# Kernel tuning notes

Hardware: AMD Instinct MI355X
Metric: run time of the kernel (lower is better)

Reference implementation:

```python
import jax, jax.numpy as jnp
import numpy as np

T, N, I, H, OUT = 16, 4096, 4, 32, 1


def setup_inputs() -> dict:
    key = jax.random.key(0)
    ks = jax.random.split(key, 12)
    f32 = jnp.float32
    x_path = jax.random.normal(ks[0], (T, N, I), f32)
    adj = jax.random.normal(ks[1], (N, N), f32) / np.float32(np.sqrt(N))
    W_enc = jax.random.normal(ks[2], (I, H), f32) / np.float32(np.sqrt(I))
    b_enc = jnp.zeros((H,), f32)
    W_gcn = jax.random.normal(ks[3], (H, H), f32) / np.float32(np.sqrt(H))
    b_gcn = jnp.zeros((H,), f32)
    W_time = jax.random.normal(ks[4], (H, H), f32) / np.float32(np.sqrt(H))
    b_time = jnp.zeros((H,), f32)
    W_proj = jax.random.normal(ks[5], (H, H * I), f32) * np.float32(0.1 / np.sqrt(H))
    b_proj = jnp.zeros((H * I,), f32)
    W_d1 = jax.random.normal(ks[6], (H, 16), f32) / np.float32(np.sqrt(H))
    b_d1 = jnp.zeros((16,), f32)
    W_d2 = jax.random.normal(ks[7], (16, OUT), f32) / np.float32(4.0)
    b_d2 = jnp.zeros((OUT,), f32)
    return dict(x_path=x_path, adj=adj, W_enc=W_enc, b_enc=b_enc,
                W_gcn=W_gcn, b_gcn=b_gcn, W_time=W_time, b_time=b_time,
                W_proj=W_proj, b_proj=b_proj, W_d1=W_d1, b_d1=b_d1,
                W_d2=W_d2, b_d2=b_d2)


def _natural_cubic_coeffs(y):
    # y: (T, C) samples on uniform grid t=0..T-1 (h=1).
    # Natural cubic spline: tridiagonal solve for second derivatives M.
    Tn = y.shape[0]
    main = jnp.ones((Tn,), y.dtype).at[1:-1].set(4.0)
    A = jnp.diag(main)
    idx = jnp.arange(1, Tn - 1)
    A = A.at[idx, idx - 1].set(1.0).at[idx, idx + 1].set(1.0)
    rhs = jnp.zeros_like(y).at[1:-1].set(6.0 * (y[2:] - 2.0 * y[1:-1] + y[:-2]))
    M = jnp.linalg.solve(A, rhs)
    b = (y[1:] - y[:-1]) - (2.0 * M[:-1] + M[1:]) / 6.0
    c = M[:-1] / 2.0
    d = (M[1:] - M[:-1]) / 6.0
    return b, c, d  # each (T-1, C); dX/dt on interval i at local s: b+2cs+3ds^2


def reference(x_path, adj, W_enc, b_enc, W_gcn, b_gcn, W_time, b_time,
              W_proj, b_proj, W_d1, b_d1, W_d2, b_d2):
    Tn, Nn, In = x_path.shape
    Hn = W_enc.shape[1]
    y = x_path.reshape(Tn, Nn * In)
    sb, sc, sd = _natural_cubic_coeffs(y)

    # z0 = encoder(X(t0)); spline value at grid point 0 equals the sample.
    z0 = x_path[0] @ W_enc + b_enc  # (N, H)

    def vf(z, dxdt):
        # SpatialVectorField + projector + block-diagonal Jacobian applied to dX/dt.
        # z: (N, H), dxdt: (N, I)
        zn = adj @ z                                     # GCN neighbor aggregation
        h = jax.nn.relu(zn @ W_gcn + b_gcn + z @ W_time + b_time)
        sens = (h @ W_proj + b_proj).reshape(Nn, Hn, In)  # per-site Jacobian blocks
        # site_identity * sens -> block-diag; matmul with dX reduces to per-site contraction
        return jnp.einsum('nhi,ni->nh', sens, dxdt)

    def rk4_step(z, coefs):
        bi, ci, di = coefs  # (N*I,)
        def dxdt(s):
            return (bi + 2.0 * ci * s + 3.0 * di * s * s).reshape(Nn, In)
        k1 = vf(z, dxdt(0.0))
        k2 = vf(z + 0.5 * k1, dxdt(0.5))
        k3 = vf(z + 0.5 * k2, dxdt(0.5))
        k4 = vf(z + k3, dxdt(1.0))
        zn = z + (k1 + 2.0 * k2 + 2.0 * k3 + k4) / 6.0
        return zn, zn

    _, zs = jax.lax.scan(rk4_step, z0, (sb, sc, sd))
    zT = jnp.concatenate([z0[None], zs], axis=0)  # (T, N, H)

    hdec = jax.nn.relu(zT @ W_d1 + b_d1)
    return jax.nn.sigmoid(hdec @ W_d2 + b_d2)  # (T, N, OUT)
```

## Files before the change

### kernel.cpp

```cpp
#include <hip/hip_runtime.h>
#include <hip/hip_bf16.h>

#define NN 4096
#define NI 16384
#define HH 32

typedef __attribute__((ext_vector_type(8))) short short8;
typedef __attribute__((ext_vector_type(4))) float f32x4;

__device__ __forceinline__ short f2bs(float f) {
  __hip_bfloat16 b = __float2bfloat16(f);
  return *(short*)&b;
}

__device__ __forceinline__ unsigned pack2(float lo, float hi) {
  return (unsigned)(unsigned short)f2bs(lo) |
         ((unsigned)(unsigned short)f2bs(hi) << 16);
}

__device__ __forceinline__ long zt_idx(int n, int h) {
  const int hb = h >> 4, hl = h & 15;
  const int kb = n >> 5, oct = (n >> 3) & 3, j = n & 7;
  return ((long)(hb * 128 + kb) * 64 + hl + 16 * oct) * 8 + j;
}

__global__ void k_spline(const float* __restrict__ x,
                         float* __restrict__ dx0, float* __restrict__ dxh,
                         float* __restrict__ dx1, unsigned* __restrict__ bar) {
  if (blockIdx.x == 0) {
    for (int i = threadIdx.x; i < 576; i += 256) bar[i] = 0u;
  }
  const int c = blockIdx.x * 256 + threadIdx.x;
  float y[16];
#pragma unroll
  for (int t = 0; t < 16; ++t) y[t] = x[t * NI + c];
  float cp[15], dp[15], M[16];
  cp[1] = 0.25f;
  dp[1] = (6.f * (y[2] - 2.f * y[1] + y[0])) * 0.25f;
#pragma unroll
  for (int i = 2; i <= 14; ++i) {
    float ri = 6.f * (y[i + 1] - 2.f * y[i] + y[i - 1]);
    float inv = 1.f / (4.f - cp[i - 1]);
    cp[i] = inv;
    dp[i] = (ri - dp[i - 1]) * inv;
  }
  M[0] = 0.f; M[15] = 0.f;
  M[14] = dp[14];
#pragma unroll
  for (int i = 13; i >= 1; --i) M[i] = dp[i] - cp[i] * M[i + 1];
#pragma unroll
  for (int i = 0; i < 15; ++i) {
    float b = (y[i + 1] - y[i]) - (2.f * M[i] + M[i + 1]) * (1.f / 6.f);
    float cc = 0.5f * M[i];
    float dd = (M[i + 1] - M[i]) * (1.f / 6.f);
    dx0[i * NI + c] = b;
    dxh[i * NI + c] = b + cc + 0.75f * dd;
    dx1[i * NI + c] = b + 2.f * cc + 3.f * dd;
  }
}

__device__ __forceinline__ void gridbar(unsigned* bar, int bid, int e) {
  __syncthreads();
  if (threadIdx.x == 0) {
    asm volatile("s_waitcnt vmcnt(0)" ::: "memory");
    unsigned old = __hip_atomic_fetch_add(bar + (bid & 7) * 32, 1u,
                                          __ATOMIC_RELAXED, __HIP_MEMORY_SCOPE_AGENT);
    if (old == (unsigned)(32 * e - 1)) {
      unsigned rr = __hip_atomic_fetch_add(bar + 256, 1u,
                                           __ATOMIC_RELAXED, __HIP_MEMORY_SCOPE_AGENT);
      if (rr == (unsigned)(8 * e - 1)) {
#pragma unroll
        for (int g = 0; g < 8; ++g)
          __hip_atomic_store(bar + 320 + g * 32, (unsigned)e,
                             __ATOMIC_RELAXED, __HIP_MEMORY_SCOPE_AGENT);
      }
    }
    while (__hip_atomic_load(bar + 320 + (bid & 7) * 32, __ATOMIC_RELAXED,
                             __HIP_MEMORY_SCOPE_AGENT) < (unsigned)e)
      __builtin_amdgcn_s_sleep(8);
    __builtin_amdgcn_fence(__ATOMIC_ACQUIRE, "agent");
  }
  __syncthreads();
}

__device__ __forceinline__ void dec_block(const float* zsrc ,
                                          const float* Wd1s ,
                                          const float* dsm, float* op,
                                          int r0, int tid) {
  if (tid < 256) {
    const int rr = tid >> 4, jj = tid & 15;
    float hv = dsm[jj];
#pragma unroll
    for (int hh = 0; hh < 32; ++hh) hv = fmaf(zsrc[rr * 33 + hh], Wd1s[hh * 16 + jj], hv);
    float val = fmaxf(hv, 0.f) * dsm[16 + jj];
#pragma unroll
    for (int off = 1; off < 16; off <<= 1) val += __shfl_xor(val, off, 64);
    if (jj == 0)
      __hip_atomic_store(op + r0 + rr, 1.f / (1.f + expf(-(dsm[32] + val))),
                         __ATOMIC_RELAXED, __HIP_MEMORY_SCOPE_AGENT);
  }
}

__global__ __launch_bounds__(1024, 4) void k_ode(
    const float* __restrict__ adj, const float* __restrict__ x,
    const float* __restrict__ dx0, const float* __restrict__ dxh,
    const float* __restrict__ dx1,
    const float* __restrict__ We, const float* __restrict__ be,
    const float* __restrict__ Wg, const float* __restrict__ bg,
    const float* __restrict__ Wt, const float* __restrict__ bt,
    const float* __restrict__ Wp, const float* __restrict__ bp,
    const float* __restrict__ Wd1, const float* __restrict__ bd1,
    const float* __restrict__ Wd2, const float* __restrict__ bd2,
    short* __restrict__ zTa, short* __restrict__ zTb,
    unsigned* __restrict__ bar, float* __restrict__ out) {
  __shared__ float red2[16][32][17];
  __shared__ float zn_s[16][33];
  __shared__ float h_s[16][33];
  __shared__ float ze_s[16][33];
  __shared__ float zb_s[16][33];
  __shared__ float ka_s[16][33];
  __shared__ float Wg_s[32][32];
  __shared__ float Wt_s[32][32];
  __shared__ float Wp_s[32][136];
  __shared__ float Wd1_s[32][16];
  __shared__ float bgt_s[32];
  __shared__ float bp_s[128];
  __shared__ float dsm[33];

  const int tid = threadIdx.x;
  const int lane = tid & 63;
  const int w = tid >> 6;
  const int bid = blockIdx.x;
  const int r0 = bid * 16;
  const int lane8 = lane * 8;
  const int fr = lane & 15, oct = lane >> 4;

  short8 av[8];
  {
    const float* arow = adj + (long)(r0 + fr) * NN + w * 256 + oct * 8;
#pragma unroll
    for (int i = 0; i < 8; ++i) {
      const float4 u0 = *(const float4*)(arow + i * 32);
      const float4 u1 = *(const float4*)(arow + i * 32 + 4);
      short8 rf;
      rf[0] = f2bs(u0.x); rf[1] = f2bs(u0.y); rf[2] = f2bs(u0.z); rf[3] = f2bs(u0.w);
      rf[4] = f2bs(u1.x); rf[5] = f2bs(u1.y); rf[6] = f2bs(u1.z); rf[7] = f2bs(u1.w);
      av[i] = rf;
    }
  }

  Wg_s[tid >> 5][tid & 31] = Wg[tid];
  Wt_s[tid >> 5][tid & 31] = Wt[tid];
#pragma unroll
  for (int idx = tid; idx < 4096; idx += 1024)
    Wp_s[idx >> 7][idx & 127] = Wp[idx];
  if (tid < 512) Wd1_s[tid >> 4][tid & 15] = Wd1[tid];
  if (tid < 32) bgt_s[tid] = bg[tid] + bt[tid];
  if (tid < 128) bp_s[tid] = bp[tid];
  if (tid < 16) { dsm[tid] = bd1[tid]; dsm[16 + tid] = Wd2[tid]; }
  if (tid == 0) dsm[32] = bd2[0];

  const int r = (tid >> 5) & 15, c = tid & 31;
  if (tid < 512) {
    const int n = r0 + r;
    float acc = be[c];
#pragma unroll
    for (int i = 0; i < 4; ++i) acc = fmaf(x[n * 4 + i], We[i * 32 + c], acc);
    zb_s[r][c] = acc;
    ze_s[r][c] = acc;
  }
  __syncthreads();
  if (tid >= 256 && tid < 512) {
    const int q = tid - 256;
    const int rr = (q >> 5) * 2, cc = q & 31;
    const unsigned pk = pack2(ze_s[rr][cc], ze_s[rr + 1][cc]);
    __hip_atomic_store((unsigned*)zTa + (zt_idx(r0 + rr, cc) >> 1), pk,
                       __ATOMIC_RELAXED, __HIP_MEMORY_SCOPE_AGENT);
  }
  dec_block(&zb_s[0][0], &Wd1_s[0][0], dsm, out, r0, tid);

  int ep = 0;
  gridbar(bar, bid, ++ep);

  const short* zi = zTa;
  short* zo = zTb;

  for (int t = 0; t < 15; ++t) {
    const float* dt0 = dx0 + t * NI;
    const float* dth = dxh + t * NI;
    const float* dt1 = dx1 + t * NI;
    for (int j = 1; j <= 4; ++j) {
      const float* dxp = (j == 1) ? dt0 : (j == 4) ? dt1 : dth;

      float4 dxv;
      if (tid < 512) dxv = *(const float4*)(dxp + (long)(r0 + r) * 4);

      f32x4 a0 = {0.f, 0.f, 0.f, 0.f}, a1 = {0.f, 0.f, 0.f, 0.f};
      const short* bp0 = zi + (w * 8) * 512 + lane8;
#pragma unroll
      for (int i = 0; i < 8; ++i) {
        const short8 b0 = *(const short8*)(bp0 + i * 512);
        const short8 b1 = *(const short8*)(bp0 + 65536 + i * 512);
        a0 = __builtin_amdgcn_mfma_f32_16x16x32_bf16(av[i], b0, a0, 0, 0, 0);
        a1 = __builtin_amdgcn_mfma_f32_16x16x32_bf16(av[i], b1, a1, 0, 0, 0);
      }
      {
        const int crow = (lane >> 4) * 4, ccol = lane & 15;
#pragma unroll
        for (int q = 0; q < 4; ++q) {
          red2[crow + q][ccol][w] = a0[q];
          red2[crow + q][ccol + 16][w] = a1[q];
        }
      }
      __syncthreads();

      if (tid < 512) {
        float zn = 0.f;
#pragma unroll
        for (int q = 0; q < 16; ++q) zn += red2[r][c][q];
        zn_s[r][c] = zn;
      }
      __syncthreads();

      if (tid < 512) {
        float hv = bgt_s[c];
#pragma unroll
        for (int kk = 0; kk < 32; ++kk)
          hv = fmaf(zn_s[r][kk], Wg_s[kk][c], fmaf(ze_s[r][kk], Wt_s[kk][c], hv));
        h_s[r][c] = fmaxf(hv, 0.f);
      }
      __syncthreads();

      if (tid < 512) {
        float s0 = bp_s[c * 4], s1 = bp_s[c * 4 + 1];
        float s2 = bp_s[c * 4 + 2], s3 = bp_s[c * 4 + 3];
#pragma unroll
        for (int hp = 0; hp < 32; ++hp) {
          const float4 wv = *(const float4*)&Wp_s[hp][c * 4];
          const float hr = h_s[r][hp];
          s0 = fmaf(hr, wv.x, s0);
          s1 = fmaf(hr, wv.y, s1);
          s2 = fmaf(hr, wv.z, s2);
          s3 = fmaf(hr, wv.w, s3);
        }
        const float kv = s0 * dxv.x + s1 * dxv.y + s2 * dxv.z + s3 * dxv.w;
        float zev;
        if (j == 1)      { ka_s[r][c] = kv;            zev = zb_s[r][c] + 0.5f * kv; }
        else if (j == 2) { ka_s[r][c] += 2.f * kv;     zev = zb_s[r][c] + 0.5f * kv; }
        else if (j == 3) { ka_s[r][c] += 2.f * kv;     zev = zb_s[r][c] + kv; }
        else { zev = zb_s[r][c] + (ka_s[r][c] + kv) * (1.f / 6.f); zb_s[r][c] = zev; }
        ze_s[r][c] = zev;
      }
      __syncthreads();

      if (tid >= 256 && tid < 512) {
        const int q = tid - 256;
        const int rr = (q >> 5) * 2, cc = q & 31;
        const unsigned pk = pack2(ze_s[rr][cc], ze_s[rr + 1][cc]);
        __hip_atomic_store((unsigned*)zo + (zt_idx(r0 + rr, cc) >> 1), pk,
                           __ATOMIC_RELAXED, __HIP_MEMORY_SCOPE_AGENT);
      }
      if (j == 4)
        dec_block(&zb_s[0][0], &Wd1_s[0][0], dsm, out + (t + 1) * NN, r0, tid);

      gridbar(bar, bid, ++ep);
      const short* tz = zi; zi = zo; zo = (short*)tz;
    }
  }
}

extern "C" void kernel_launch(void* const* d_in, const int* in_sizes, int n_in,
                              void* d_out, int out_size, void* d_ws, size_t ws_size,
                              hipStream_t stream) {
  (void)in_sizes; (void)n_in; (void)out_size; (void)ws_size;
  const float* x      = (const float*)d_in[0];
  const float* adj    = (const float*)d_in[1];
  const float* W_enc  = (const float*)d_in[2];
  const float* b_enc  = (const float*)d_in[3];
  const float* W_gcn  = (const float*)d_in[4];
  const float* b_gcn  = (const float*)d_in[5];
  const float* W_time = (const float*)d_in[6];
  const float* b_time = (const float*)d_in[7];
  const float* W_proj = (const float*)d_in[8];
  const float* b_proj = (const float*)d_in[9];
  const float* W_d1   = (const float*)d_in[10];
  const float* b_d1   = (const float*)d_in[11];
  const float* W_d2   = (const float*)d_in[12];
  const float* b_d2   = (const float*)d_in[13];
  float* out = (float*)d_out;

  float* dx0 = (float*)d_ws;
  float* dxh = dx0 + 15 * NI;
  float* dx1 = dxh + 15 * NI;
  short* zTa = (short*)(dx1 + 15 * NI);
  short* zTb = zTa + HH * NN;
  unsigned* bar = (unsigned*)(zTb + HH * NN);

  k_spline<<<64, 256, 0, stream>>>(x, dx0, dxh, dx1, bar);

  void* args[] = {(void*)&adj, (void*)&x, (void*)&dx0, (void*)&dxh, (void*)&dx1,
                  (void*)&W_enc, (void*)&b_enc, (void*)&W_gcn, (void*)&b_gcn,
                  (void*)&W_time, (void*)&b_time, (void*)&W_proj, (void*)&b_proj,
                  (void*)&W_d1, (void*)&b_d1, (void*)&W_d2, (void*)&b_d2,
                  (void*)&zTa, (void*)&zTb, (void*)&bar, (void*)&out};
  hipError_t err = hipLaunchCooperativeKernel((const void*)k_ode, dim3(256),
                                              dim3(1024), args, 0, stream);
  if (err != hipSuccess) {
    k_ode<<<256, 1024, 0, stream>>>(adj, x, dx0, dxh, dx1, W_enc, b_enc,
                                    W_gcn, b_gcn, W_time, b_time, W_proj, b_proj,
                                    W_d1, b_d1, W_d2, b_d2, zTa, zTb, bar, out);
  }
}
```

Measured before the change: 760.3 us.

## Drop barrier fences and use agent-scope atomic loads for z exchange

The grid barrier no longer waits on vmcnt(0) or issues an acquire fence, and its spin sleep is shortened. To keep cross-block visibility, the z exchange buffer is now read with relaxed agent-scope 64-bit atomic loads and written with 64-bit atomic stores packing four rows each. The MFMA loop is split into two load-then-compute halves, and the reduction buffer padding is changed. This cuts barrier latency per RK stage. It relies on relaxed atomics for ordering instead of fences, which risks memory-ordering races.

Result: no change. 753.1 us (median of 2 runs) (-1.0%).

```diff
diff --git a/kernel.cpp b/kernel.cpp
--- a/kernel.cpp
+++ b/kernel.cpp
@@ -7,6 +7,9 @@
 
 typedef __attribute__((ext_vector_type(8))) short short8;
 typedef __attribute__((ext_vector_type(4))) float f32x4;
+typedef unsigned long long u64;
+
+union bfrag { short8 s8; u64 q[2]; };
 
 __device__ __forceinline__ short f2bs(float f) {
   __hip_bfloat16 b = __float2bfloat16(f);
@@ -62,7 +65,6 @@
 __device__ __forceinline__ void gridbar(unsigned* bar, int bid, int e) {
   __syncthreads();
   if (threadIdx.x == 0) {
-    asm volatile("s_waitcnt vmcnt(0)" ::: "memory");
     unsigned old = __hip_atomic_fetch_add(bar + (bid & 7) * 32, 1u,
                                           __ATOMIC_RELAXED, __HIP_MEMORY_SCOPE_AGENT);
     if (old == (unsigned)(32 * e - 1)) {
@@ -77,8 +79,7 @@
     }
     while (__hip_atomic_load(bar + 320 + (bid & 7) * 32, __ATOMIC_RELAXED,
                              __HIP_MEMORY_SCOPE_AGENT) < (unsigned)e)
-      __builtin_amdgcn_s_sleep(8);
-    __builtin_amdgcn_fence(__ATOMIC_ACQUIRE, "agent");
+      __builtin_amdgcn_s_sleep(2);
   }
   __syncthreads();
 }
@@ -113,7 +114,7 @@
     const float* __restrict__ Wd2, const float* __restrict__ bd2,
     short* __restrict__ zTa, short* __restrict__ zTb,
     unsigned* __restrict__ bar, float* __restrict__ out) {
-  __shared__ float red2[16][32][17];
+  __shared__ float red2[16][34][17];
   __shared__ float zn_s[16][33];
   __shared__ float h_s[16][33];
   __shared__ float ze_s[16][33];
@@ -132,7 +133,6 @@
   const int w = tid >> 6;
   const int bid = blockIdx.x;
   const int r0 = bid * 16;
-  const int lane8 = lane * 8;
   const int fr = lane & 15, oct = lane >> 4;
 
   short8 av[8];
@@ -170,11 +170,12 @@
     ze_s[r][c] = acc;
   }
   __syncthreads();
-  if (tid >= 256 && tid < 512) {
+  if (tid >= 256 && tid < 384) {
     const int q = tid - 256;
-    const int rr = (q >> 5) * 2, cc = q & 31;
-    const unsigned pk = pack2(ze_s[rr][cc], ze_s[rr + 1][cc]);
-    __hip_atomic_store((unsigned*)zTa + (zt_idx(r0 + rr, cc) >> 1), pk,
+    const int cc = q & 31, rr = (q >> 5) * 4;
+    const u64 pk = (u64)pack2(ze_s[rr][cc], ze_s[rr + 1][cc]) |
+                   ((u64)pack2(ze_s[rr + 2][cc], ze_s[rr + 3][cc]) << 32);
+    __hip_atomic_store((u64*)zTa + (zt_idx(r0 + rr, cc) >> 2), pk,
                        __ATOMIC_RELAXED, __HIP_MEMORY_SCOPE_AGENT);
   }
   dec_block(&zb_s[0][0], &Wd1_s[0][0], dsm, out, r0, tid);
@@ -196,14 +197,29 @@
       if (tid < 512) dxv = *(const float4*)(dxp + (long)(r0 + r) * 4);
 
       f32x4 a0 = {0.f, 0.f, 0.f, 0.f}, a1 = {0.f, 0.f, 0.f, 0.f};
-      const short* bp0 = zi + (w * 8) * 512 + lane8;
+      const u64* bq = (const u64*)zi + (size_t)w * 1024 + (lane << 1);
+      bfrag bf[8];
 #pragma unroll
       for (int i = 0; i < 8; ++i) {
-        const short8 b0 = *(const short8*)(bp0 + i * 512);
-        const short8 b1 = *(const short8*)(bp0 + 65536 + i * 512);
-        a0 = __builtin_amdgcn_mfma_f32_16x16x32_bf16(av[i], b0, a0, 0, 0, 0);
-        a1 = __builtin_amdgcn_mfma_f32_16x16x32_bf16(av[i], b1, a1, 0, 0, 0);
-      }
+        bf[i].q[0] = __hip_atomic_load(bq + i * 128,
+                                       __ATOMIC_RELAXED, __HIP_MEMORY_SCOPE_AGENT);
+        bf[i].q[1] = __hip_atomic_load(bq + i * 128 + 1,
+                                       __ATOMIC_RELAXED, __HIP_MEMORY_SCOPE_AGENT);
+      }
+#pragma unroll
+      for (int i = 0; i < 8; ++i)
+        a0 = __builtin_amdgcn_mfma_f32_16x16x32_bf16(av[i], bf[i].s8, a0, 0, 0, 0);
+#pragma unroll
+      for (int i = 0; i < 8; ++i) {
+        bf[i].q[0] = __hip_atomic_load(bq + 16384 + i * 128,
+                                       __ATOMIC_RELAXED, __HIP_MEMORY_SCOPE_AGENT);
+        bf[i].q[1] = __hip_atomic_load(bq + 16384 + i * 128 + 1,
+                                       __ATOMIC_RELAXED, __HIP_MEMORY_SCOPE_AGENT);
+      }
+#pragma unroll
+      for (int i = 0; i < 8; ++i)
+        a1 = __builtin_amdgcn_mfma_f32_16x16x32_bf16(av[i], bf[i].s8, a1, 0, 0, 0);
+
       {
         const int crow = (lane >> 4) * 4, ccol = lane & 15;
 #pragma unroll
@@ -253,11 +269,12 @@
       }
       __syncthreads();
 
-      if (tid >= 256 && tid < 512) {
+      if (tid >= 256 && tid < 384) {
         const int q = tid - 256;
-        const int rr = (q >> 5) * 2, cc = q & 31;
-        const unsigned pk = pack2(ze_s[rr][cc], ze_s[rr + 1][cc]);
-        __hip_atomic_store((unsigned*)zo + (zt_idx(r0 + rr, cc) >> 1), pk,
+        const int cc = q & 31, rr = (q >> 5) * 4;
+        const u64 pk = (u64)pack2(ze_s[rr][cc], ze_s[rr + 1][cc]) |
+                       ((u64)pack2(ze_s[rr + 2][cc], ze_s[rr + 3][cc]) << 32);
+        __hip_atomic_store((u64*)zo + (zt_idx(r0 + rr, cc) >> 2), pk,
                            __ATOMIC_RELAXED, __HIP_MEMORY_SCOPE_AGENT);
       }
       if (j == 4)
```
